# Performance work log

Hardware: AMD Instinct MI355X
Metric: run time of the kernel (lower is better)

## Reference

```python
import jax, jax.numpy as jnp
import numpy as np

B, T, D = 2, 2048, 1024
H = 16
DH = D // H            # 64, per-head dim
C = 128                # d_kv_compress
ROPE_BASE = 10000.0


def _rope_cos_sin(t_len, d_head, dtype):
    # freqs: (T, d_head/2); emb = cat(freqs, freqs) -> (T, d_head)
    inv_freq = 1.0 / (ROPE_BASE ** (jnp.arange(0, d_head, 2, dtype=jnp.float32) / d_head))
    freqs = jnp.arange(t_len, dtype=jnp.float32)[:, None] * inv_freq[None, :]
    emb = jnp.concatenate([freqs, freqs], axis=-1)
    return jnp.cos(emb).astype(dtype), jnp.sin(emb).astype(dtype)


def _rotate_half(x):
    x1, x2 = jnp.split(x, 2, axis=-1)
    return jnp.concatenate([-x2, x1], axis=-1)


def _apply_rope(x, cos, sin):
    # x: (B,H,T,DH); cos/sin: (T,DH)
    return x * cos[None, None] + _rotate_half(x) * sin[None, None]


def setup_inputs() -> dict:
    key = jax.random.key(0)
    ks = jax.random.split(key, 12)
    s = 0.02
    return {
        "x": jax.random.normal(ks[0], (B, T, D), dtype=jnp.float32),
        "w_dk": jax.random.normal(ks[1], (D, C), dtype=jnp.float32) * s,
        "b_dk": jnp.zeros((C,), dtype=jnp.float32),
        "w_dv": jax.random.normal(ks[2], (D, C), dtype=jnp.float32) * s,
        "b_dv": jnp.zeros((C,), dtype=jnp.float32),
        "w_uk": jax.random.normal(ks[3], (C, D), dtype=jnp.float32) * s,
        "b_uk": jnp.zeros((D,), dtype=jnp.float32),
        "w_uv": jax.random.normal(ks[4], (C, D), dtype=jnp.float32) * s,
        "b_uv": jnp.zeros((D,), dtype=jnp.float32),
        "w_o": jax.random.normal(ks[5], (D, D), dtype=jnp.float32) * s,
        "b_o": jnp.zeros((D,), dtype=jnp.float32),
    }


def reference(x, w_dk, b_dk, w_dv, b_dv, w_uk, b_uk, w_uv, b_uv, w_o, b_o):
    Bx, Tx, Dx = x.shape
    # low-rank KV compression then up-projection
    c_k = x @ w_dk + b_dk                      # (B,T,C)
    c_v = x @ w_dv + b_dv                      # (B,T,C)
    k = c_k @ w_uk + b_uk                      # (B,T,D)
    v = c_v @ w_uv + b_uv                      # (B,T,D)

    def split_heads(t):  # (B,T,D) -> (B,H,T,DH)
        return t.reshape(Bx, Tx, H, DH).transpose(0, 2, 1, 3)

    q = split_heads(x)
    k = split_heads(k)
    v = split_heads(v)

    cos, sin = _rope_cos_sin(Tx, DH, x.dtype)
    q = _apply_rope(q, cos, sin)
    k = _apply_rope(k, cos, sin)

    scale = 1.0 / np.sqrt(DH)
    attn = jnp.einsum('bhid,bhjd->bhij', q, k) * scale
    attn = jax.nn.softmax(attn, axis=-1)
    out = jnp.einsum('bhij,bhjd->bhid', attn, v)   # (B,H,T,DH)
    out = out.transpose(0, 2, 1, 3).reshape(Bx, Tx, Dx)
    return out @ w_o + b_o
```

## Files before the change

### kernel.cpp

```cpp
#include <hip/hip_runtime.h>
#include <hip/hip_bf16.h>
#include <math.h>

constexpr int kB  = 2;
constexpr int kT  = 2048;
constexpr int kD  = 1024;
constexpr int kH  = 16;
constexpr int kDH = 64;
constexpr int kC  = 128;
constexpr int kM  = kB * kT;
constexpr int kBH = kB * kH;

#define LOG10000_OVER_32 0.28782313662425575f
#define QSCALE 0.1803368801111773f

typedef unsigned short ushort_t;
using short8 = __attribute__((ext_vector_type(8))) short;
using f32x4  = __attribute__((ext_vector_type(4))) float;

__device__ inline ushort_t f2bf(float f) {
    __hip_bfloat16 h = __float2bfloat16(f);
    return *reinterpret_cast<ushort_t*>(&h);
}

__device__ inline short8 cvt8(const float* p) {
    float4 f0 = *reinterpret_cast<const float4*>(p);
    float4 f1 = *reinterpret_cast<const float4*>(p + 4);
    short8 v;
    v[0] = (short)f2bf(f0.x); v[1] = (short)f2bf(f0.y);
    v[2] = (short)f2bf(f0.z); v[3] = (short)f2bf(f0.w);
    v[4] = (short)f2bf(f1.x); v[5] = (short)f2bf(f1.y);
    v[6] = (short)f2bf(f1.z); v[7] = (short)f2bf(f1.w);
    return v;
}

__global__ __launch_bounds__(256)
void wtrans(const float* __restrict__ w_dk, const float* __restrict__ w_dv,
            const float* __restrict__ w_uk, const float* __restrict__ w_uv,
            const float* __restrict__ w_o,
            ushort_t* __restrict__ dkT, ushort_t* __restrict__ dvT,
            ushort_t* __restrict__ ukT, ushort_t* __restrict__ uvT,
            ushort_t* __restrict__ oT, float2* __restrict__ tab) {
    if (blockIdx.z == 5) {
        int flat = blockIdx.y * 32 + blockIdx.x;
        if (flat >= kT / 8) return;
        int t = flat * 8 + (threadIdx.x >> 5);
        int i = threadIdx.x & 31;
        float inv_freq = expf(-(float)i * LOG10000_OVER_32);
        float s, c;
        sincosf((float)t * inv_freq, &s, &c);
        tab[t * 32 + i] = make_float2(c, s);
        return;
    }
    const float* src; ushort_t* dst; int R, C;
    switch (blockIdx.z) {
        case 0: src = w_dk; dst = dkT; R = kD; C = kC; break;
        case 1: src = w_dv; dst = dvT; R = kD; C = kC; break;
        case 2: src = w_uk; dst = ukT; R = kC; C = kD; break;
        case 3: src = w_uv; dst = uvT; R = kC; C = kD; break;
        default: src = w_o; dst = oT;  R = kD; C = kD; break;
    }
    int c0 = blockIdx.x * 32, r0 = blockIdx.y * 32;
    if (c0 >= C || r0 >= R) return;

    __shared__ float Tl[32][33];
    int tx = threadIdx.x & 31, ty = threadIdx.x >> 5;
#pragma unroll
    for (int i = 0; i < 4; ++i)
        Tl[ty + 8 * i][tx] = src[(size_t)(r0 + ty + 8 * i) * C + c0 + tx];
    __syncthreads();
#pragma unroll
    for (int i = 0; i < 4; ++i)
        dst[(size_t)(c0 + ty + 8 * i) * R + r0 + tx] = f2bf(Tl[tx][ty + 8 * i]);
}

template<int MODE0, int MODE1>
__global__ __launch_bounds__(256)
void gemm_mfma(const ushort_t* __restrict__ A0_, const ushort_t* __restrict__ A1_,
               const ushort_t* __restrict__ Wt0, const float* __restrict__ bias0, void* __restrict__ C0,
               const ushort_t* __restrict__ Wt1, const float* __restrict__ bias1, void* __restrict__ C1,
               const float2* __restrict__ tab, int M, int N, int K) {
    constexpr int LDT = 40;
    __shared__ __align__(16) ushort_t As[128 * LDT];
    __shared__ __align__(16) ushort_t Bs[128 * LDT];

    const ushort_t* A    = blockIdx.z ? A1_ : A0_;
    const ushort_t* Wt   = blockIdx.z ? Wt1 : Wt0;
    const float*    bias = blockIdx.z ? bias1 : bias0;
    void*           Cc   = blockIdx.z ? C1 : C0;
    const int       mode = blockIdx.z ? MODE1 : MODE0;

    const int tid  = threadIdx.x;
    const int wave = tid >> 6, lane = tid & 63;
    const int g = lane >> 4, cl = lane & 15;
    const int m0 = blockIdx.y * 128, n0 = blockIdx.x * 128;
    const int wm = (wave >> 1) * 64, wn = (wave & 1) * 64;

    const int ar = tid >> 1;
    const int ac = (tid & 1) * 16;

    f32x4 acc[4][4] = {};

    for (int k0 = 0; k0 < K; k0 += 32) {
        {
            const ushort_t* Ab = A + (size_t)(m0 + ar) * K + k0 + ac;
            *reinterpret_cast<short8*>(&As[ar * LDT + ac])     = *reinterpret_cast<const short8*>(Ab);
            *reinterpret_cast<short8*>(&As[ar * LDT + ac + 8]) = *reinterpret_cast<const short8*>(Ab + 8);
            const ushort_t* Wb = Wt + (size_t)(n0 + ar) * K + k0 + ac;
            *reinterpret_cast<short8*>(&Bs[ar * LDT + ac])     = *reinterpret_cast<const short8*>(Wb);
            *reinterpret_cast<short8*>(&Bs[ar * LDT + ac + 8]) = *reinterpret_cast<const short8*>(Wb + 8);
        }
        __syncthreads();

        short8 a[4], b[4];
#pragma unroll
        for (int mi = 0; mi < 4; ++mi)
            a[mi] = *reinterpret_cast<const short8*>(&As[(wm + mi * 16 + cl) * LDT + g * 8]);
#pragma unroll
        for (int ni = 0; ni < 4; ++ni)
            b[ni] = *reinterpret_cast<const short8*>(&Bs[(wn + ni * 16 + cl) * LDT + g * 8]);
#pragma unroll
        for (int mi = 0; mi < 4; ++mi)
#pragma unroll
            for (int ni = 0; ni < 4; ++ni)
                acc[mi][ni] = __builtin_amdgcn_mfma_f32_16x16x32_bf16(a[mi], b[ni], acc[mi][ni], 0, 0, 0);
        __syncthreads();
    }

#pragma unroll
    for (int mi = 0; mi < 4; ++mi) {
        if (mode == 4) {
            const int h = (n0 + wn) >> 6;
#pragma unroll
            for (int r = 0; r < 4; ++r) {
                const int m = m0 + wm + mi * 16 + 4 * g + r;
                const int bb = m >> 11, t = m & (kT - 1);
                ushort_t* kp = (ushort_t*)Cc + (((size_t)bb * kH + h) * kT + t) * kDH;
#pragma unroll
                for (int pr = 0; pr < 2; ++pr) {
                    const int i = pr * 16 + cl;
                    float2 cs = tab[t * 32 + i];
                    float v1 = acc[mi][pr][r]     + bias[n0 + wn + pr * 16 + cl];
                    float v2 = acc[mi][pr + 2][r] + bias[n0 + wn + (pr + 2) * 16 + cl];
                    kp[i]      = f2bf(v1 * cs.x - v2 * cs.y);
                    kp[i + 32] = f2bf(v2 * cs.x + v1 * cs.y);
                }
            }
        } else {
#pragma unroll
            for (int ni = 0; ni < 4; ++ni) {
                const int mb = m0 + wm + mi * 16 + 4 * g;
                const int nn = n0 + wn + ni * 16 + cl;
                const float bv = bias[nn];
                const int h = nn >> 6, d = nn & (kDH - 1);
                const int bb = mb >> 11, t0 = mb & (kT - 1);
                uint2 u;
                u.x = (unsigned int)f2bf(acc[mi][ni][0] + bv) | ((unsigned int)f2bf(acc[mi][ni][1] + bv) << 16);
                u.y = (unsigned int)f2bf(acc[mi][ni][2] + bv) | ((unsigned int)f2bf(acc[mi][ni][3] + bv) << 16);
                ushort_t* vt = (ushort_t*)Cc;
                *reinterpret_cast<uint2*>(&vt[(((size_t)bb * kH + h) * kDH + d) * kT + t0]) = u;
            }
        }
    }
}

template<bool AF32, int MODE>
__global__ __launch_bounds__(256)
void gemm64(const void* __restrict__ A0_, const void* __restrict__ A1_,
            const ushort_t* __restrict__ Wt0, const float* __restrict__ bias0, void* __restrict__ C0,
            const ushort_t* __restrict__ Wt1, const float* __restrict__ bias1, void* __restrict__ C1,
            int M, int N, int K) {
    constexpr int LDT = 40;
    __shared__ __align__(16) ushort_t As[128 * LDT];
    __shared__ __align__(16) ushort_t Bs[64 * LDT];

    const void*     A    = blockIdx.z ? A1_ : A0_;
    const ushort_t* Wt   = blockIdx.z ? Wt1 : Wt0;
    const float*    bias = blockIdx.z ? bias1 : bias0;
    void*           Cc   = blockIdx.z ? C1 : C0;

    const int tid  = threadIdx.x;
    const int wave = tid >> 6, lane = tid & 63;
    const int g = lane >> 4, cl = lane & 15;
    const int m0 = blockIdx.y * 128, n0 = blockIdx.x * 64;
    const int wm = (wave >> 1) * 64, wn = (wave & 1) * 32;

    const int ar = tid >> 1, ac = (tid & 1) * 16;
    const int br = tid >> 2, bc = (tid & 3) * 8;

    f32x4 acc[4][2] = {};

    for (int k0 = 0; k0 < K; k0 += 32) {
        if constexpr (AF32) {
            const float* Af = (const float*)A + (size_t)(m0 + ar) * K + k0 + ac;
            *reinterpret_cast<short8*>(&As[ar * LDT + ac])     = cvt8(Af);
            *reinterpret_cast<short8*>(&As[ar * LDT + ac + 8]) = cvt8(Af + 8);
        } else {
            const ushort_t* Ab = (const ushort_t*)A + (size_t)(m0 + ar) * K + k0 + ac;
            *reinterpret_cast<short8*>(&As[ar * LDT + ac])     = *reinterpret_cast<const short8*>(Ab);
            *reinterpret_cast<short8*>(&As[ar * LDT + ac + 8]) = *reinterpret_cast<const short8*>(Ab + 8);
        }
        *reinterpret_cast<short8*>(&Bs[br * LDT + bc]) =
            *reinterpret_cast<const short8*>(Wt + (size_t)(n0 + br) * K + k0 + bc);
        __syncthreads();

        short8 a[4], b[2];
#pragma unroll
        for (int mi = 0; mi < 4; ++mi)
            a[mi] = *reinterpret_cast<const short8*>(&As[(wm + mi * 16 + cl) * LDT + g * 8]);
#pragma unroll
        for (int ni = 0; ni < 2; ++ni)
            b[ni] = *reinterpret_cast<const short8*>(&Bs[(wn + ni * 16 + cl) * LDT + g * 8]);
#pragma unroll
        for (int mi = 0; mi < 4; ++mi)
#pragma unroll
            for (int ni = 0; ni < 2; ++ni)
                acc[mi][ni] = __builtin_amdgcn_mfma_f32_16x16x32_bf16(a[mi], b[ni], acc[mi][ni], 0, 0, 0);
        __syncthreads();
    }

#pragma unroll
    for (int mi = 0; mi < 4; ++mi)
#pragma unroll
        for (int ni = 0; ni < 2; ++ni) {
            const int mb = m0 + wm + mi * 16 + 4 * g;
            const int nn = n0 + wn + ni * 16 + cl;
            const float bv = bias[nn];
            if constexpr (MODE == 0) {
#pragma unroll
                for (int r = 0; r < 4; ++r)
                    ((float*)Cc)[(size_t)(mb + r) * N + nn] = acc[mi][ni][r] + bv;
            } else {
#pragma unroll
                for (int r = 0; r < 4; ++r)
                    ((ushort_t*)Cc)[(size_t)(mb + r) * N + nn] = f2bf(acc[mi][ni][r] + bv);
            }
        }
}

__global__ __launch_bounds__(256)
void attn_mfma(const float* __restrict__ x, const float2* __restrict__ tab,
               const ushort_t* __restrict__ k_bf, const ushort_t* __restrict__ vt_bf,
               ushort_t* __restrict__ att_bf) {
    constexpr int LDP = 36;
    const int blk  = blockIdx.x;
    const int bh   = (blk & 7) * 4 + ((blk >> 3) & 3);
    const int qt   = blk >> 5;
    const int tid  = threadIdx.x;
    const int wave = tid >> 6, lane = tid & 63;
    const int g = lane >> 4, c = lane & 15;
    const int qbase = qt * 64 + wave * 16;
    const int b = bh >> 4, h = bh & (kH - 1);

    __shared__ __align__(16) ushort_t Ks[32 * 64];
    __shared__ __align__(16) ushort_t Vs[64 * 32];
    __shared__ __align__(16) ushort_t P_lds[4][16 * LDP];
    ushort_t* P = P_lds[wave];

    short8 qa0, qa1;
    {
        const int t = qbase + c;
        const float* xp = x + ((size_t)(b * kT + t)) * kD + h * kDH + g * 8;
        float xa[8], xb[8]; float2 cs[8];
        *reinterpret_cast<float4*>(&xa[0]) = *reinterpret_cast<const float4*>(xp);
        *reinterpret_cast<float4*>(&xa[4]) = *reinterpret_cast<const float4*>(xp + 4);
        *reinterpret_cast<float4*>(&xb[0]) = *reinterpret_cast<const float4*>(xp + 32);
        *reinterpret_cast<float4*>(&xb[4]) = *reinterpret_cast<const float4*>(xp + 36);
        const float2* tp = tab + (size_t)t * 32 + g * 8;
#pragma unroll
        for (int j = 0; j < 8; j += 2)
            *reinterpret_cast<float4*>(&cs[j]) = *reinterpret_cast<const float4*>(tp + j);
#pragma unroll
        for (int j = 0; j < 8; ++j) {
            qa0[j] = (short)f2bf((xa[j] * cs[j].x - xb[j] * cs[j].y) * QSCALE);
            qa1[j] = (short)f2bf((xb[j] * cs[j].x + xa[j] * cs[j].y) * QSCALE);
        }
    }

    const ushort_t* kb = k_bf + (size_t)bh * kT * kDH;
    const ushort_t* vb = vt_bf + (size_t)bh * kDH * kT;

    const int kr_ = tid >> 3, kc_ = (tid & 7) * 8;
    const int ksw = kr_ * 64 + (kc_ ^ ((kr_ & 7) << 3));
    const int vr_ = tid >> 2, vc_ = (tid & 3) * 8;

    f32x4 acc[4] = {};
    float lsum[4] = {};

    for (int kt = 0; kt < kT; kt += 32) {
        *reinterpret_cast<short8*>(&Ks[ksw]) =
            *reinterpret_cast<const short8*>(&kb[(size_t)(kt + kr_) * kDH + kc_]);
        *reinterpret_cast<short8*>(&Vs[vr_ * 32 + vc_]) =
            *reinterpret_cast<const short8*>(&vb[(size_t)vr_ * kT + kt + vc_]);
        __syncthreads();

        short8 kf[2][2];
#pragma unroll
        for (int kj = 0; kj < 2; ++kj)
#pragma unroll
            for (int f = 0; f < 2; ++f) {
                const int row = kj * 16 + c;
                const int col = f * 32 + g * 8;
                kf[kj][f] = *reinterpret_cast<const short8*>(
                    &Ks[row * 64 + (col ^ ((row & 7) << 3))]);
            }

        f32x4 z = {0.f, 0.f, 0.f, 0.f};
        f32x4 s0 = __builtin_amdgcn_mfma_f32_16x16x32_bf16(qa0, kf[0][0], z, 0, 0, 0);
        s0 = __builtin_amdgcn_mfma_f32_16x16x32_bf16(qa1, kf[0][1], s0, 0, 0, 0);
        f32x4 s1 = __builtin_amdgcn_mfma_f32_16x16x32_bf16(qa0, kf[1][0], z, 0, 0, 0);
        s1 = __builtin_amdgcn_mfma_f32_16x16x32_bf16(qa1, kf[1][1], s1, 0, 0, 0);

#pragma unroll
        for (int r = 0; r < 4; ++r) {
            float p0 = exp2f(s0[r]);
            float p1 = exp2f(s1[r]);
            lsum[r] += p0 + p1;
            P[(4 * g + r) * LDP + c]      = f2bf(p0);
            P[(4 * g + r) * LDP + 16 + c] = f2bf(p1);
        }
        short8 pa = *reinterpret_cast<const short8*>(&P[c * LDP + g * 8]);

        short8 vf[4];
#pragma unroll
        for (int n = 0; n < 4; ++n)
            vf[n] = *reinterpret_cast<const short8*>(&Vs[(16 * n + c) * 32 + g * 8]);
#pragma unroll
        for (int n = 0; n < 4; ++n)
            acc[n] = __builtin_amdgcn_mfma_f32_16x16x32_bf16(pa, vf[n], acc[n], 0, 0, 0);
        __syncthreads();
    }

#pragma unroll
    for (int off = 1; off < 16; off <<= 1)
#pragma unroll
        for (int r = 0; r < 4; ++r)
            lsum[r] += __shfl_xor(lsum[r], off, 64);

#pragma unroll
    for (int r = 0; r < 4; ++r) {
        float inv_l = 1.0f / lsum[r];
        size_t row = (size_t)(b * kT + qbase + 4 * g + r) * kD + h * kDH;
#pragma unroll
        for (int n = 0; n < 4; ++n)
            att_bf[row + 16 * n + c] = f2bf(acc[n][r] * inv_l);
    }
}

extern "C" void kernel_launch(void* const* d_in, const int* in_sizes, int n_in,
                              void* d_out, int out_size, void* d_ws, size_t ws_size,
                              hipStream_t stream) {
    const float* x    = (const float*)d_in[0];
    const float* w_dk = (const float*)d_in[1];
    const float* b_dk = (const float*)d_in[2];
    const float* w_dv = (const float*)d_in[3];
    const float* b_dv = (const float*)d_in[4];
    const float* w_uk = (const float*)d_in[5];
    const float* b_uk = (const float*)d_in[6];
    const float* w_uv = (const float*)d_in[7];
    const float* b_uv = (const float*)d_in[8];
    const float* w_o  = (const float*)d_in[9];
    const float* b_o  = (const float*)d_in[10];
    float* out = (float*)d_out;

    char* w = (char*)d_ws;
    ushort_t* k_bf   = (ushort_t*)w;  w += (size_t)kM * kD * 2;
    ushort_t* vt_bf  = (ushort_t*)w;  w += (size_t)kM * kD * 2;
    ushort_t* att_bf = (ushort_t*)w;  w += (size_t)kM * kD * 2;
    ushort_t* ckbf   = (ushort_t*)w;  w += (size_t)kM * kC * 2;
    ushort_t* cvbf   = (ushort_t*)w;  w += (size_t)kM * kC * 2;
    ushort_t* dkT    = (ushort_t*)w;  w += (size_t)kC * kD * 2;
    ushort_t* dvT    = (ushort_t*)w;  w += (size_t)kC * kD * 2;
    ushort_t* ukT    = (ushort_t*)w;  w += (size_t)kD * kC * 2;
    ushort_t* uvT    = (ushort_t*)w;  w += (size_t)kD * kC * 2;
    ushort_t* oT     = (ushort_t*)w;  w += (size_t)kD * kD * 2;
    float2*   tab    = (float2*)w;    w += (size_t)kT * 32 * 8;

    dim3 blk(256);

    wtrans<<<dim3(32, 32, 6), blk, 0, stream>>>(w_dk, w_dv, w_uk, w_uv, w_o,
                                                dkT, dvT, ukT, uvT, oT, tab);

    gemm64<true, 3><<<dim3(kC / 64, kM / 128, 2), blk, 0, stream>>>(
        x, x, dkT, b_dk, ckbf, dvT, b_dv, cvbf, kM, kC, kD);

    gemm_mfma<4, 2><<<dim3(kD / 128, kM / 128, 2), blk, 0, stream>>>(
        ckbf, cvbf, ukT, b_uk, k_bf, uvT, b_uv, vt_bf, tab, kM, kD, kC);

    attn_mfma<<<dim3(kT / 64 * kBH), blk, 0, stream>>>(x, tab, k_bf, vt_bf, att_bf);

    gemm64<false, 0><<<dim3(kD / 64, kM / 128, 1), blk, 0, stream>>>(
        att_bf, att_bf, oT, b_o, out, oT, b_o, out, kM, kD, kD);
}
```

Baseline: 251.7 us.

## Split attention over KV halves with partial-sum combine and separate Q RoPE kernel

The attention kernel now splits the key range into two halves, doubling the block count. Each half writes unnormalized fp32 partial outputs and row sums, and a new combine kernel merges them into the bf16 attention output. Q RoPE is moved into a separate pre-pass that writes head-major bf16 Q, and the V tile in shared memory gets a padded stride to reduce bank conflicts. The aim is more parallelism across the GPU, at the cost of two extra launches and extra fp32 global traffic. Because scores are not max-subtracted, summing the halves stays exact.

```diff
diff --git a/kernel.cpp b/kernel.cpp
--- a/kernel.cpp
+++ b/kernel.cpp
@@ -239,43 +239,47 @@
 }
 
 __global__ __launch_bounds__(256)
-void attn_mfma(const float* __restrict__ x, const float2* __restrict__ tab,
-               const ushort_t* __restrict__ k_bf, const ushort_t* __restrict__ vt_bf,
-               ushort_t* __restrict__ att_bf) {
+void rope_split_q(const float* __restrict__ x, const float2* __restrict__ tab,
+                  ushort_t* __restrict__ q_bf) {
+    int idx = blockIdx.x * 256 + threadIdx.x;
+    int i = idx & 31;
+    int h = (idx >> 5) & (kH - 1);
+    int t = (idx >> 9) & (kT - 1);
+    int b = idx >> 20;
+
+    const float* xp = x + ((size_t)(b * kT + t)) * kD + h * kDH;
+    float x1 = xp[i];
+    float x2 = xp[i + 32];
+    float2 cs = tab[t * 32 + i];
+
+    ushort_t* qp = q_bf + (((size_t)(b * kH + h)) * kT + t) * kDH;
+    qp[i]      = f2bf((x1 * cs.x - x2 * cs.y) * QSCALE);
+    qp[i + 32] = f2bf((x2 * cs.x + x1 * cs.y) * QSCALE);
+}
+
+__global__ __launch_bounds__(256)
+void attn_mfma(const ushort_t* __restrict__ q_bf, const ushort_t* __restrict__ k_bf,
+               const ushort_t* __restrict__ vt_bf,
+               float* __restrict__ pacc, float* __restrict__ pl) {
+    constexpr int LDV = 40;
     constexpr int LDP = 36;
     const int blk  = blockIdx.x;
     const int bh   = (blk & 7) * 4 + ((blk >> 3) & 3);
-    const int qt   = blk >> 5;
+    const int half = (blk >> 5) & 1;
+    const int qt   = blk >> 6;
     const int tid  = threadIdx.x;
     const int wave = tid >> 6, lane = tid & 63;
     const int g = lane >> 4, c = lane & 15;
     const int qbase = qt * 64 + wave * 16;
-    const int b = bh >> 4, h = bh & (kH - 1);
 
     __shared__ __align__(16) ushort_t Ks[32 * 64];
-    __shared__ __align__(16) ushort_t Vs[64 * 32];
+    __shared__ __align__(16) ushort_t Vs[64 * LDV];
     __shared__ __align__(16) ushort_t P_lds[4][16 * LDP];
     ushort_t* P = P_lds[wave];
 
-    short8 qa0, qa1;
-    {
-        const int t = qbase + c;
-        const float* xp = x + ((size_t)(b * kT + t)) * kD + h * kDH + g * 8;
-        float xa[8], xb[8]; float2 cs[8];
-        *reinterpret_cast<float4*>(&xa[0]) = *reinterpret_cast<const float4*>(xp);
-        *reinterpret_cast<float4*>(&xa[4]) = *reinterpret_cast<const float4*>(xp + 4);
-        *reinterpret_cast<float4*>(&xb[0]) = *reinterpret_cast<const float4*>(xp + 32);
-        *reinterpret_cast<float4*>(&xb[4]) = *reinterpret_cast<const float4*>(xp + 36);
-        const float2* tp = tab + (size_t)t * 32 + g * 8;
-#pragma unroll
-        for (int j = 0; j < 8; j += 2)
-            *reinterpret_cast<float4*>(&cs[j]) = *reinterpret_cast<const float4*>(tp + j);
-#pragma unroll
-        for (int j = 0; j < 8; ++j) {
-            qa0[j] = (short)f2bf((xa[j] * cs[j].x - xb[j] * cs[j].y) * QSCALE);
-            qa1[j] = (short)f2bf((xb[j] * cs[j].x + xa[j] * cs[j].y) * QSCALE);
-        }
-    }
+    const ushort_t* qp = q_bf + ((size_t)bh * kT + qbase) * kDH;
+    short8 qa0 = *reinterpret_cast<const short8*>(qp + (size_t)c * kDH + g * 8);
+    short8 qa1 = *reinterpret_cast<const short8*>(qp + (size_t)c * kDH + g * 8 + 32);
 
     const ushort_t* kb = k_bf + (size_t)bh * kT * kDH;
     const ushort_t* vb = vt_bf + (size_t)bh * kDH * kT;
@@ -287,10 +291,11 @@
     f32x4 acc[4] = {};
     float lsum[4] = {};
 
-    for (int kt = 0; kt < kT; kt += 32) {
+    const int kt0 = half * (kT / 2);
+    for (int kt = kt0; kt < kt0 + kT / 2; kt += 32) {
         *reinterpret_cast<short8*>(&Ks[ksw]) =
             *reinterpret_cast<const short8*>(&kb[(size_t)(kt + kr_) * kDH + kc_]);
-        *reinterpret_cast<short8*>(&Vs[vr_ * 32 + vc_]) =
+        *reinterpret_cast<short8*>(&Vs[vr_ * LDV + vc_]) =
             *reinterpret_cast<const short8*>(&vb[(size_t)vr_ * kT + kt + vc_]);
         __syncthreads();
 
@@ -324,7 +329,7 @@
         short8 vf[4];
 #pragma unroll
         for (int n = 0; n < 4; ++n)
-            vf[n] = *reinterpret_cast<const short8*>(&Vs[(16 * n + c) * 32 + g * 8]);
+            vf[n] = *reinterpret_cast<const short8*>(&Vs[(16 * n + c) * LDV + g * 8]);
 #pragma unroll
         for (int n = 0; n < 4; ++n)
             acc[n] = __builtin_amdgcn_mfma_f32_16x16x32_bf16(pa, vf[n], acc[n], 0, 0, 0);
@@ -339,12 +344,38 @@
 
 #pragma unroll
     for (int r = 0; r < 4; ++r) {
-        float inv_l = 1.0f / lsum[r];
-        size_t row = (size_t)(b * kT + qbase + 4 * g + r) * kD + h * kDH;
+        size_t row = ((size_t)(half * kBH + bh) * kT + qbase + 4 * g + r) * kDH;
 #pragma unroll
         for (int n = 0; n < 4; ++n)
-            att_bf[row + 16 * n + c] = f2bf(acc[n][r] * inv_l);
-    }
+            pacc[row + 16 * n + c] = acc[n][r];
+    }
+    if (c == 0) {
+#pragma unroll
+        for (int r = 0; r < 4; ++r)
+            pl[(size_t)(half * kBH + bh) * kT + qbase + 4 * g + r] = lsum[r];
+    }
+}
+
+__global__ __launch_bounds__(256)
+void attn_combine(const float* __restrict__ pacc, const float* __restrict__ pl,
+                  ushort_t* __restrict__ att_bf) {
+    int flat = blockIdx.x * 256 + threadIdx.x;
+    int d4 = (flat & 15) * 4;
+    int t  = (flat >> 4) & (kT - 1);
+    int bh = flat >> 15;
+    int b = bh >> 4, h = bh & (kH - 1);
+
+    size_t i0 = ((size_t)bh * kT + t) * kDH + d4;
+    size_t i1 = ((size_t)(kBH + bh) * kT + t) * kDH + d4;
+    float4 a0 = *reinterpret_cast<const float4*>(&pacc[i0]);
+    float4 a1 = *reinterpret_cast<const float4*>(&pacc[i1]);
+    float inv = 1.0f / (pl[(size_t)bh * kT + t] + pl[(size_t)(kBH + bh) * kT + t]);
+
+    uint2 u;
+    u.x = (unsigned int)f2bf((a0.x + a1.x) * inv) | ((unsigned int)f2bf((a0.y + a1.y) * inv) << 16);
+    u.y = (unsigned int)f2bf((a0.z + a1.z) * inv) | ((unsigned int)f2bf((a0.w + a1.w) * inv) << 16);
+    ushort_t* op = att_bf + ((size_t)(b * kT + t)) * kD + h * kDH + d4;
+    *reinterpret_cast<uint2*>(op) = u;
 }
 
 extern "C" void kernel_launch(void* const* d_in, const int* in_sizes, int n_in,
@@ -364,9 +395,9 @@
     float* out = (float*)d_out;
 
     char* w = (char*)d_ws;
+    ushort_t* q_bf   = (ushort_t*)w;  w += (size_t)kM * kD * 2;
     ushort_t* k_bf   = (ushort_t*)w;  w += (size_t)kM * kD * 2;
     ushort_t* vt_bf  = (ushort_t*)w;  w += (size_t)kM * kD * 2;
-    ushort_t* att_bf = (ushort_t*)w;  w += (size_t)kM * kD * 2;
     ushort_t* ckbf   = (ushort_t*)w;  w += (size_t)kM * kC * 2;
     ushort_t* cvbf   = (ushort_t*)w;  w += (size_t)kM * kC * 2;
     ushort_t* dkT    = (ushort_t*)w;  w += (size_t)kC * kD * 2;
@@ -375,6 +406,8 @@
     ushort_t* uvT    = (ushort_t*)w;  w += (size_t)kD * kC * 2;
     ushort_t* oT     = (ushort_t*)w;  w += (size_t)kD * kD * 2;
     float2*   tab    = (float2*)w;    w += (size_t)kT * 32 * 8;
+    float*    pacc   = (float*)w;     w += (size_t)2 * kBH * kT * kDH * 4;
+    float*    pl     = (float*)w;     w += (size_t)2 * kBH * kT * 4;
 
     dim3 blk(256);
 
@@ -387,8 +420,12 @@
     gemm_mfma<4, 2><<<dim3(kD / 128, kM / 128, 2), blk, 0, stream>>>(
         ckbf, cvbf, ukT, b_uk, k_bf, uvT, b_uv, vt_bf, tab, kM, kD, kC);
 
-    attn_mfma<<<dim3(kT / 64 * kBH), blk, 0, stream>>>(x, tab, k_bf, vt_bf, att_bf);
+    rope_split_q<<<(kB * kT * kH * 32) / 256, blk, 0, stream>>>(x, tab, q_bf);
+
+    attn_mfma<<<dim3(kT / 64 * kBH * 2), blk, 0, stream>>>(q_bf, k_bf, vt_bf, pacc, pl);
+
+    attn_combine<<<dim3(kBH * kT * kDH / (4 * 256)), blk, 0, stream>>>(pacc, pl, q_bf);
 
     gemm64<false, 0><<<dim3(kD / 64, kM / 128, 1), blk, 0, stream>>>(
-        att_bf, att_bf, oT, b_o, out, oT, b_o, out, kM, kD, kD);
-}
+        q_bf, q_bf, oT, b_o, out, oT, b_o, out, kM, kD, kD);
+}
```

After: 256.2 us. No clear change (+1.8%).
